# Performance work log

Hardware: AMD Instinct MI355X
Metric: run time of the kernel (lower is better)

Reference implementation:

```python
import jax, jax.numpy as jnp
import numpy as np

K = 16          # neighbors per query (args.k)
EPS_NORM = 1e-5  # LayerNorm / BatchNorm eps (torch default)


def _knn_edges(xyz, B, n):
    # batch-aware kNN: equal-sized batches, edges never cross batch boundary
    x = xyz.reshape(B, n, 3)
    d2 = jnp.sum((x[:, :, None, :] - x[:, None, :, :]) ** 2, -1)   # [B,n,n]
    _, idx = jax.lax.top_k(-d2, K)                                 # [B,n,K] local neighbor ids
    col = (idx + (jnp.arange(B) * n)[:, None, None]).reshape(-1)   # source (neighbor) [E]
    row = jnp.repeat(jnp.arange(B * n), K)                         # target (query)    [E]
    return row, col


def _forward(support_xyz, batch_index, features, lang_features, mask_flattened,
             W1, b1, ln_g, ln_b, W2, b2,
             Wl1, bl1, bn_g, bn_b, Wl2, bl2,
             Wr1, br1, Wr2, br2, row, col):
    N = support_xyz.shape[0]
    B, L, Fl = lang_features.shape
    # feat_encoder: Linear -> LayerNorm -> ReLU -> Linear
    h = features @ W1 + b1
    mu = h.mean(-1, keepdims=True)
    var = ((h - mu) ** 2).mean(-1, keepdims=True)
    h = (h - mu) / jnp.sqrt(var + EPS_NORM) * ln_g + ln_b
    feats = jax.nn.relu(h) @ W2 + b2                               # [N,F]
    # lang_encoder: Linear -> BatchNorm1d (batch statistics) -> ReLU -> Linear
    hl = lang_features.reshape(B * L, Fl) @ Wl1 + bl1
    mul = hl.mean(0)
    varl = ((hl - mul) ** 2).mean(0)
    hl = (hl - mul) / jnp.sqrt(varl + EPS_NORM) * bn_g + bn_b
    lang = (jax.nn.relu(hl) @ Wl2 + bl2).reshape(B, L, -1)         # [B,L,F]
    lang_flat = lang[batch_index]                                  # [N,L,F]
    # per-point / per-token attention logits
    atten = jnp.einsum('nf,nlf->nl', feats, lang_flat)             # [N,L]
    # segment softmax over incoming kNN edges (CenterOp max / add)
    attenmax = jax.ops.segment_max(atten[col], row, num_segments=N, indices_are_sorted=True)
    a = jnp.exp(atten[col] - attenmax[row])                        # [E,L]
    attensum = jax.ops.segment_sum(a, row, num_segments=N, indices_are_sorted=True)
    # CenterConv message
    att = a / attensum[row] * mask_flattened[row]                  # [E,L]
    att = att / (att.sum(-1, keepdims=True) + 1e-7)
    ctx = jnp.einsum('el,elf->ef', att, lang_flat[col])            # [E,F] attended lang feat
    xi, xj = support_xyz[row], support_xyz[col]
    d = xi - xj
    nrm = jnp.sqrt(jnp.sum(d * d, -1, keepdims=True) + 1e-12)
    ew = jnp.concatenate([xi, xj, d, nrm], -1)                     # [E,10]
    ew = jax.nn.relu(ew @ Wr1 + br1) @ Wr2 + br2                   # [E,F] rel_encoder
    msg = feats[col] * ctx * ew                                    # [E,F]
    rel = jax.ops.segment_sum(msg, row, num_segments=N, indices_are_sorted=True)
    return feats + rel


def setup_inputs() -> dict:
    key = jax.random.key(0)
    ks = jax.random.split(key, 12)
    B, n, L = 4, 1024, 16
    N = B * n
    Fv, Fl, F = 256, 768, 128
    def w(k, shp, fan):
        return jax.random.normal(k, shp, jnp.float32) / np.sqrt(fan).astype(np.float32)
    mask = (jax.random.uniform(ks[3], (N, L)) < 0.8).astype(jnp.float32).at[:, 0].set(1.0)
    return {
        'support_xyz': jax.random.normal(ks[0], (N, 3), jnp.float32),
        'batch_index': jnp.repeat(jnp.arange(B), n),
        'features': jax.random.normal(ks[1], (N, Fv), jnp.float32),
        'lang_features': jax.random.normal(ks[2], (B, L, Fl), jnp.float32),
        'mask_flattened': mask,
        'W1': w(ks[4], (Fv, F), Fv), 'b1': jnp.zeros(F, jnp.float32),
        'ln_g': jnp.ones(F, jnp.float32), 'ln_b': jnp.zeros(F, jnp.float32),
        'W2': w(ks[5], (F, F), F), 'b2': jnp.zeros(F, jnp.float32),
        'Wl1': w(ks[6], (Fl, F), Fl), 'bl1': jnp.zeros(F, jnp.float32),
        'bn_g': jnp.ones(F, jnp.float32), 'bn_b': jnp.zeros(F, jnp.float32),
        'Wl2': w(ks[7], (F, F), F), 'bl2': jnp.zeros(F, jnp.float32),
        'Wr1': w(ks[8], (10, 64), 10), 'br1': jnp.zeros(64, jnp.float32),
        'Wr2': w(ks[9], (64, F), 64), 'br2': jnp.zeros(F, jnp.float32),
    }


def reference(support_xyz, batch_index, features, lang_features, mask_flattened,
              W1, b1, ln_g, ln_b, W2, b2,
              Wl1, bl1, bn_g, bn_b, Wl2, bl2,
              Wr1, br1, Wr2, br2):
    B = lang_features.shape[0]
    n = support_xyz.shape[0] // B
    row, col = _knn_edges(support_xyz, B, n)
    return _forward(support_xyz, batch_index, features, lang_features, mask_flattened,
                    W1, b1, ln_g, ln_b, W2, b2,
                    Wl1, bl1, bn_g, bn_b, Wl2, bl2,
                    Wr1, br1, Wr2, br2, row, col)
```

## Files before the change

kernel.cpp:

```cpp
#include <hip/hip_runtime.h>

typedef unsigned long long u64;
typedef unsigned int u32;
typedef short short8 __attribute__((ext_vector_type(8)));
typedef float f32x4 __attribute__((ext_vector_type(4)));
typedef u32 u32x4v __attribute__((ext_vector_type(4)));

#define N_PTS   4096
#define B_SZ    4
#define L_TOK   16
#define FV      256
#define FL      768
#define FDIM    128
#define KNN     16
#define RH      64

#define MFMA_BF16(a, b, c) __builtin_amdgcn_mfma_f32_16x16x32_bf16((a), (b), (c), 0, 0, 0)

__device__ __forceinline__ short f2bf(float f) {
    unsigned int x = __float_as_uint(f);
    unsigned int r = (x + 0x7fffu + ((x >> 16) & 1u)) >> 16;
    return (short)r;
}

__device__ __forceinline__ u32 splitf(float f) {
    u32 bits = __float_as_uint(f);
    u32 hi = bits >> 16;
    float lof = f - __uint_as_float(bits & 0xffff0000u);
    u32 lo = __float_as_uint(lof) >> 16;
    return (hi << 16) | lo;
}

__global__ __launch_bounds__(256) void k1_kernel(const float* __restrict__ xyz,
                                                 const float* __restrict__ lf,
                                                 const float* __restrict__ Wl1,
                                                 const float* __restrict__ bl1,
                                                 const float* __restrict__ W1,
                                                 const float* __restrict__ W2,
                                                 const float* __restrict__ Wr2,
                                                 int* __restrict__ knn,
                                                 float* __restrict__ hl,
                                                 short* __restrict__ w1p_hi,
                                                 short* __restrict__ w1p_lo,
                                                 short* __restrict__ w2p_hi,
                                                 short* __restrict__ w2p_lo,
                                                 short* __restrict__ w2pe) {
    __shared__ float smem[3072];
    int b = blockIdx.x, t = threadIdx.x;
    int wid = t >> 6, lane = t & 63;
    int e = lane & 15, q = lane >> 4;

    if (b < 1024) {
        int base = ((b * 4) >> 10) << 10;
        for (int idx = t; idx < 3072; idx += 256) smem[idx] = xyz[base * 3 + idx];
        __syncthreads();
        int qi = b * 4 + wid;
        int ql = qi - base;
        float qx = smem[ql * 3 + 0];
        float qy = smem[ql * 3 + 1];
        float qz = smem[ql * 3 + 2];
        double key[16];
#pragma unroll
        for (int m = 0; m < 16; m++) {
            int jl = lane + (m << 6);
            float dx = qx - smem[jl * 3 + 0];
            float dy = qy - smem[jl * 3 + 1];
            float dz = qz - smem[jl * 3 + 2];
            float d2 = __fadd_rn(__fadd_rn(__fmul_rn(dx, dx), __fmul_rn(dy, dy)),
                                 __fmul_rn(dz, dz));
            key[m] = (double)__float_as_uint(d2) * 1024.0 + (double)jl;
        }
#pragma unroll
        for (int k = 2; k <= 16; k <<= 1) {
#pragma unroll
            for (int jj = k >> 1; jj > 0; jj >>= 1) {
#pragma unroll
                for (int i = 0; i < 16; i++) {
                    int l = i ^ jj;
                    if (l > i) {
                        double lo = fmin(key[i], key[l]);
                        double hi = fmax(key[i], key[l]);
                        bool asc = ((i & k) == 0);
                        key[i] = asc ? lo : hi;
                        key[l] = asc ? hi : lo;
                    }
                }
            }
        }
#pragma unroll
        for (int lvl = 1; lvl <= 32; lvl <<= 1) {
            double pk[16];
#pragma unroll
            for (int i = 0; i < 16; i++) pk[i] = __shfl_xor(key[15 - i], lvl, 64);
#pragma unroll
            for (int i = 0; i < 16; i++) key[i] = fmin(key[i], pk[i]);
            if (lvl != 32) {
#pragma unroll
                for (int jj = 8; jj > 0; jj >>= 1) {
#pragma unroll
                    for (int i = 0; i < 16; i++) {
                        int l = i ^ jj;
                        if (l > i) {
                            double lo = fmin(key[i], key[l]);
                            double hi = fmax(key[i], key[l]);
                            key[i] = lo;
                            key[l] = hi;
                        }
                    }
                }
            }
        }
        if (lane == 0) {
            int idx[16];
#pragma unroll
            for (int i = 0; i < 16; i++)
                idx[i] = base + (int)(((u64)key[i]) & 1023u);
#pragma unroll
            for (int w = 0; w < 4; w++) {
                int4 v = {idx[4 * w], idx[4 * w + 1], idx[4 * w + 2], idx[4 * w + 3]};
                *(int4*)&knn[qi * KNN + 4 * w] = v;
            }
        }
    } else if (b < 1088) {
        int r = b - 1024;
        float* lrow = smem;
        float* part = smem + 768;
        for (int k = t; k < FL; k += 256) lrow[k] = lf[r * FL + k];
        __syncthreads();
        int c = t & 127, kh = t >> 7;
        float acc = (kh == 0) ? bl1[c] : 0.f;
        int k0 = kh * 384;
        for (int k = k0; k < k0 + 384; k++) acc += lrow[k] * Wl1[k * FDIM + c];
        part[kh * FDIM + c] = acc;
        __syncthreads();
        if (kh == 0) hl[r * FDIM + c] = part[c] + part[FDIM + c];
    } else if (b < 1100) {
        int isW2 = (b >= 1096);
        int ks = isW2 ? (b - 1096) : (b - 1088);
        const float* W = isW2 ? W2 : W1;
        short* ph = isW2 ? w2p_hi : w1p_hi;
        short* pl = isW2 ? w2p_lo : w1p_lo;
#pragma unroll
        for (int p = 0; p < 2; p++) {
            int ct = wid * 2 + p;
            short8 hi, lo;
#pragma unroll
            for (int j = 0; j < 8; j++) {
                u32 pr = splitf(W[(ks * 32 + q * 8 + j) * FDIM + ct * 16 + e]);
                hi[j] = (short)(pr >> 16);
                lo[j] = (short)(pr & 0xffffu);
            }
            int o = ((ks * 8 + ct) * 64 + lane) * 8;
            *(short8*)(ph + o) = hi;
            *(short8*)(pl + o) = lo;
        }
    } else {
        int ks = b - 1100;
#pragma unroll
        for (int p = 0; p < 2; p++) {
            int ct = wid * 2 + p;
            short8 v;
#pragma unroll
            for (int j = 0; j < 8; j++)
                v[j] = f2bf(Wr2[(ks * 32 + q * 8 + j) * FDIM + ct * 16 + e]);
            *(short8*)(w2pe + ((ks * 8 + ct) * 64 + lane) * 8) = v;
        }
    }
}

__global__ __launch_bounds__(256) void k2_kernel(const float* __restrict__ features,
                                                 const short* __restrict__ w1p_hi,
                                                 const short* __restrict__ w1p_lo,
                                                 const short* __restrict__ w2p_hi,
                                                 const short* __restrict__ w2p_lo,
                                                 const float* __restrict__ b1,
                                                 const float* __restrict__ ln_g,
                                                 const float* __restrict__ ln_b,
                                                 const float* __restrict__ b2,
                                                 const float* __restrict__ hl,
                                                 const float* __restrict__ bn_g,
                                                 const float* __restrict__ bn_b,
                                                 const float* __restrict__ Wl2,
                                                 const float* __restrict__ bl2,
                                                 float* __restrict__ feats,
                                                 float* __restrict__ lang) {
    __shared__ u32 smem_u[8448];
    int b = blockIdx.x, t = threadIdx.x;
    int wid = t >> 6, lane = t & 63;
    int e = lane & 15, q = lane >> 4;
    if (b < 64) {
        int rt = b * 4 + wid;
        f32x4 acc[8];
#pragma unroll
        for (int ct = 0; ct < 8; ct++) {
            float v = b1[ct * 16 + e];
            acc[ct] = (f32x4){v, v, v, v};
        }
        for (int ks = 0; ks < 8; ks++) {
            const float* src = features + (rt * 16 + e) * FV + ks * 32 + q * 8;
            float4 f0 = *(const float4*)src;
            float4 f1 = *(const float4*)(src + 4);
            float av[8] = {f0.x, f0.y, f0.z, f0.w, f1.x, f1.y, f1.z, f1.w};
            short8 ah, al;
#pragma unroll
            for (int j = 0; j < 8; j++) {
                u32 pr = splitf(av[j]);
                ah[j] = (short)(pr >> 16);
                al[j] = (short)(pr & 0xffffu);
            }
#pragma unroll
            for (int ct = 0; ct < 8; ct++) {
                int bo = ((ks * 8 + ct) * 64 + lane) * 8;
                short8 bh = *(const short8*)(w1p_hi + bo);
                short8 bl = *(const short8*)(w1p_lo + bo);
                acc[ct] = MFMA_BF16(ah, bh, acc[ct]);
                acc[ct] = MFMA_BF16(al, bh, acc[ct]);
                acc[ct] = MFMA_BF16(ah, bl, acc[ct]);
            }
        }
        float s[4], sq[4];
#pragma unroll
        for (int r = 0; r < 4; r++) { s[r] = 0.f; sq[r] = 0.f; }
#pragma unroll
        for (int ct = 0; ct < 8; ct++)
#pragma unroll
            for (int r = 0; r < 4; r++) {
                float v = acc[ct][r];
                s[r] += v; sq[r] += v * v;
            }
#pragma unroll
        for (int off = 1; off < 16; off <<= 1)
#pragma unroll
            for (int r = 0; r < 4; r++) {
                s[r] += __shfl_xor(s[r], off, 16);
                sq[r] += __shfl_xor(sq[r], off, 16);
            }
        float mu[4], rs[4];
#pragma unroll
        for (int r = 0; r < 4; r++) {
            mu[r] = s[r] * (1.f / 128.f);
            float var = sq[r] * (1.f / 128.f) - mu[r] * mu[r];
            rs[r] = rsqrtf(var + 1e-5f);
        }
        u32* hrow = smem_u + wid * (16 * 132);
#pragma unroll
        for (int ct = 0; ct < 8; ct++) {
            float g = ln_g[ct * 16 + e], bb = ln_b[ct * 16 + e];
#pragma unroll
            for (int r = 0; r < 4; r++) {
                float n = fmaxf((acc[ct][r] - mu[r]) * rs[r] * g + bb, 0.f);
                hrow[(q * 4 + r) * 132 + ct * 16 + e] = splitf(n);
            }
        }
        f32x4 acc2[8];
#pragma unroll
        for (int ct = 0; ct < 8; ct++) {
            float v = b2[ct * 16 + e];
            acc2[ct] = (f32x4){v, v, v, v};
        }
#pragma unroll
        for (int ks = 0; ks < 4; ks++) {
            u32 hv[8];
            *(u32x4v*)&hv[0] = *(const u32x4v*)&hrow[e * 132 + ks * 32 + q * 8];
            *(u32x4v*)&hv[4] = *(const u32x4v*)&hrow[e * 132 + ks * 32 + q * 8 + 4];
            short8 ah, al;
#pragma unroll
            for (int j = 0; j < 8; j++) {
                ah[j] = (short)(hv[j] >> 16);
                al[j] = (short)(hv[j] & 0xffffu);
            }
#pragma unroll
            for (int ct = 0; ct < 8; ct++) {
                int bo = ((ks * 8 + ct) * 64 + lane) * 8;
                short8 bh = *(const short8*)(w2p_hi + bo);
                short8 bl = *(const short8*)(w2p_lo + bo);
                acc2[ct] = MFMA_BF16(ah, bh, acc2[ct]);
                acc2[ct] = MFMA_BF16(al, bh, acc2[ct]);
                acc2[ct] = MFMA_BF16(ah, bl, acc2[ct]);
            }
        }
#pragma unroll
        for (int ct = 0; ct < 8; ct++)
#pragma unroll
            for (int r = 0; r < 4; r++)
                feats[(rt * 16 + q * 4 + r) * FDIM + ct * 16 + e] = acc2[ct][r];
    } else {
        float* rl4 = (float*)smem_u;
        int tt = t & 127;
        int act = (t < 128);
        int r0 = (b - 64) * 4;
        if (act) {
            float s = 0.f, s2 = 0.f;
            for (int r = 0; r < 64; r++) {
                float v = hl[r * FDIM + tt];
                s += v; s2 += v * v;
            }
            float mu = s * (1.f / 64.f);
            float var = s2 * (1.f / 64.f) - mu * mu;
            float rs = rsqrtf(var + 1e-5f);
            float g = bn_g[tt], bb = bn_b[tt];
#pragma unroll
            for (int p = 0; p < 4; p++)
                rl4[p * FDIM + tt] = fmaxf((hl[(r0 + p) * FDIM + tt] - mu) * rs * g + bb, 0.f);
        }
        __syncthreads();
        if (act) {
            float bv = bl2[tt];
            float a0 = bv, a1 = bv, a2 = bv, a3 = bv;
            for (int k = 0; k < FDIM; k++) {
                float w = Wl2[k * FDIM + tt];
                a0 += rl4[0 * FDIM + k] * w;
                a1 += rl4[1 * FDIM + k] * w;
                a2 += rl4[2 * FDIM + k] * w;
                a3 += rl4[3 * FDIM + k] * w;
            }
            lang[(r0 + 0) * FDIM + tt] = a0;
            lang[(r0 + 1) * FDIM + tt] = a1;
            lang[(r0 + 2) * FDIM + tt] = a2;
            lang[(r0 + 3) * FDIM + tt] = a3;
        }
    }
}

__global__ __launch_bounds__(256) void atten_kernel(const float* __restrict__ feats,
                                                    const float* __restrict__ lang,
                                                    float* __restrict__ atten,
                                                    short* __restrict__ langp) {
    int b = blockIdx.x, t = threadIdx.x;
    int wid = t >> 6, lane = t & 63;
    int e = lane & 15, q = lane >> 4;
    if (b < 64) {
        int pt0 = (b * 4 + wid) * 16;
        int bi = pt0 >> 10;
        const float* arow = feats + (pt0 + e) * FDIM;
        const float* brow = lang + (bi * L_TOK + e) * FDIM;
        f32x4 acc = {0.f, 0.f, 0.f, 0.f};
#pragma unroll
        for (int ks = 0; ks < 4; ks++) {
            int off = ks * 32 + q * 8;
            float4 a0 = *(const float4*)(arow + off);
            float4 a1 = *(const float4*)(arow + off + 4);
            float4 c0 = *(const float4*)(brow + off);
            float4 c1 = *(const float4*)(brow + off + 4);
            float av[8] = {a0.x, a0.y, a0.z, a0.w, a1.x, a1.y, a1.z, a1.w};
            float bv[8] = {c0.x, c0.y, c0.z, c0.w, c1.x, c1.y, c1.z, c1.w};
            short8 ah, al, bh, bl;
#pragma unroll
            for (int j = 0; j < 8; j++) {
                u32 pa = splitf(av[j]);
                u32 pb = splitf(bv[j]);
                ah[j] = (short)(pa >> 16);
                al[j] = (short)(pa & 0xffffu);
                bh[j] = (short)(pb >> 16);
                bl[j] = (short)(pb & 0xffffu);
            }
            acc = MFMA_BF16(ah, bh, acc);
            acc = MFMA_BF16(al, bh, acc);
            acc = MFMA_BF16(ah, bl, acc);
        }
#pragma unroll
        for (int r = 0; r < 4; r++)
            atten[(pt0 + q * 4 + r) * L_TOK + e] = acc[r];
    } else {
        int bi = b - 64;
#pragma unroll
        for (int p = 0; p < 2; p++) {
            int tile = wid * 2 + p;
            short8 v;
            if (q < 2) {
#pragma unroll
                for (int j = 0; j < 8; j++)
                    v[j] = f2bf(lang[bi * L_TOK * FDIM + (q * 8 + j) * FDIM + tile * 16 + e]);
            } else {
#pragma unroll
                for (int j = 0; j < 8; j++) v[j] = 0;
            }
            *(short8*)(langp + ((bi * 8 + tile) * 64 + lane) * 8) = v;
        }
    }
}

__global__ __launch_bounds__(256) void edge_kernel(const float* __restrict__ xyz,
                                                   const float* __restrict__ mask,
                                                   const float* __restrict__ Wr1,
                                                   const float* __restrict__ br1,
                                                   const float* __restrict__ br2,
                                                   const int* __restrict__ knn,
                                                   const short* __restrict__ w2pe,
                                                   const short* __restrict__ langp,
                                                   const float* __restrict__ feats,
                                                   const float* __restrict__ atten,
                                                   float* __restrict__ out) {
    int lane = threadIdx.x & 63;
    int wid  = threadIdx.x >> 6;
    int i    = blockIdx.x * 4 + wid;
    int bi   = i >> 10;
    int quad = lane >> 4;
    int e16  = lane & 15;

    int idxe = knn[i * KNN + e16];

    float sat[8];
    if (quad < 2) {
        const float4* ap = (const float4*)(atten + idxe * L_TOK + quad * 8);
        float4 a0 = ap[0], a1 = ap[1];
        sat[0] = a0.x; sat[1] = a0.y; sat[2] = a0.z; sat[3] = a0.w;
        sat[4] = a1.x; sat[5] = a1.y; sat[6] = a1.z; sat[7] = a1.w;
    } else {
#pragma unroll
        for (int j = 0; j < 8; j++) sat[j] = 0.f;
    }

    float mx[8];
#pragma unroll
    for (int j = 0; j < 8; j++) mx[j] = sat[j];
#pragma unroll
    for (int off = 1; off < 16; off <<= 1) {
#pragma unroll
        for (int j = 0; j < 8; j++) mx[j] = fmaxf(mx[j], __shfl_xor(mx[j], off, 16));
    }
    float ex[8], sm[8];
#pragma unroll
    for (int j = 0; j < 8; j++) { ex[j] = __expf(sat[j] - mx[j]); sm[j] = ex[j]; }
#pragma unroll
    for (int off = 1; off < 16; off <<= 1) {
#pragma unroll
        for (int j = 0; j < 8; j++) sm[j] += __shfl_xor(sm[j], off, 16);
    }
    float st[8];
    if (quad < 2) {
        const float4* mp = (const float4*)(mask + i * L_TOK + quad * 8);
        float4 m0 = mp[0], m1 = mp[1];
        float mv[8] = {m0.x, m0.y, m0.z, m0.w, m1.x, m1.y, m1.z, m1.w};
#pragma unroll
        for (int j = 0; j < 8; j++) st[j] = ex[j] * (mv[j] / sm[j]);
    } else {
#pragma unroll
        for (int j = 0; j < 8; j++) st[j] = 0.f;
    }
    float s = st[0] + st[1] + st[2] + st[3] + st[4] + st[5] + st[6] + st[7];
    s += __shfl_xor(s, 16, 64);
    s += __shfl_xor(s, 32, 64);
    float inv2 = 1.f / (s + 1e-7f);
    short8 sattA;
#pragma unroll
    for (int j = 0; j < 8; j++) sattA[j] = f2bf(st[j] * inv2);

    float xi0 = xyz[i * 3 + 0], xi1 = xyz[i * 3 + 1], xi2 = xyz[i * 3 + 2];
    float xj0 = xyz[idxe * 3 + 0], xj1 = xyz[idxe * 3 + 1], xj2 = xyz[idxe * 3 + 2];
    float d0 = xi0 - xj0, d1 = xi1 - xj1, d2v = xi2 - xj2;
    float nr = sqrtf(d0 * d0 + d1 * d1 + d2v * d2v + 1e-12f);
    float ein[10] = {xi0, xi1, xi2, xj0, xj1, xj2, d0, d1, d2v, nr};
    short8 hidA[2];
#pragma unroll
    for (int sstep = 0; sstep < 2; sstep++) {
        int k0 = sstep * 32 + quad * 8;
        float h[8];
        const float4* bp = (const float4*)(br1 + k0);
        float4 b0 = bp[0], b1v = bp[1];
        h[0] = b0.x; h[1] = b0.y; h[2] = b0.z; h[3] = b0.w;
        h[4] = b1v.x; h[5] = b1v.y; h[6] = b1v.z; h[7] = b1v.w;
#pragma unroll
        for (int m = 0; m < 10; m++) {
            const float4* wp = (const float4*)(Wr1 + m * RH + k0);
            float4 w0 = wp[0], w1 = wp[1];
            float em = ein[m];
            h[0] += em * w0.x; h[1] += em * w0.y; h[2] += em * w0.z; h[3] += em * w0.w;
            h[4] += em * w1.x; h[5] += em * w1.y; h[6] += em * w1.z; h[7] += em * w1.w;
        }
#pragma unroll
        for (int j = 0; j < 8; j++) hidA[sstep][j] = f2bf(fmaxf(h[j], 0.f));
    }

    int idxr[4];
#pragma unroll
    for (int r = 0; r < 4; r++) idxr[r] = knn[i * KNN + quad * 4 + r];

#pragma unroll 2
    for (int tile = 0; tile < 8; tile++) {
        int cc = tile * 16 + e16;
        f32x4 accew = {0.f, 0.f, 0.f, 0.f};
#pragma unroll
        for (int sstep = 0; sstep < 2; sstep++) {
            short8 w2B = *(const short8*)(w2pe + ((sstep * 8 + tile) * 64 + lane) * 8);
            accew = MFMA_BF16(hidA[sstep], w2B, accew);
        }
        short8 lsB = *(const short8*)(langp + ((bi * 8 + tile) * 64 + lane) * 8);
        f32x4 accctx = {0.f, 0.f, 0.f, 0.f};
        accctx = MFMA_BF16(sattA, lsB, accctx);

        float br2c = br2[cc];
        float msum = 0.f;
#pragma unroll
        for (int r = 0; r < 4; r++) {
            float fj = feats[idxr[r] * FDIM + cc];
            msum += fj * accctx[r] * (accew[r] + br2c);
        }
        msum += __shfl_xor(msum, 16, 64);
        msum += __shfl_xor(msum, 32, 64);
        if (lane < 16)
            out[i * FDIM + cc] = feats[i * FDIM + cc] + msum;
    }
}

extern "C" void kernel_launch(void* const* d_in, const int* in_sizes, int n_in,
                              void* d_out, int out_size, void* d_ws, size_t ws_size,
                              hipStream_t stream) {
    const float* xyz   = (const float*)d_in[0];
    const float* features = (const float*)d_in[2];
    const float* lang_f   = (const float*)d_in[3];
    const float* mask     = (const float*)d_in[4];
    const float* W1   = (const float*)d_in[5];
    const float* b1   = (const float*)d_in[6];
    const float* ln_g = (const float*)d_in[7];
    const float* ln_b = (const float*)d_in[8];
    const float* W2   = (const float*)d_in[9];
    const float* b2   = (const float*)d_in[10];
    const float* Wl1  = (const float*)d_in[11];
    const float* bl1  = (const float*)d_in[12];
    const float* bn_g = (const float*)d_in[13];
    const float* bn_b = (const float*)d_in[14];
    const float* Wl2  = (const float*)d_in[15];
    const float* bl2  = (const float*)d_in[16];
    const float* Wr1  = (const float*)d_in[17];
    const float* br1  = (const float*)d_in[18];
    const float* Wr2  = (const float*)d_in[19];
    const float* br2  = (const float*)d_in[20];

    float* ws_feats = (float*)d_ws;
    float* ws_atten = ws_feats + N_PTS * FDIM;
    float* ws_lang  = ws_atten + N_PTS * L_TOK;
    float* ws_hl    = ws_lang + B_SZ * L_TOK * FDIM;
    int*   ws_knn   = (int*)(ws_hl + 64 * FDIM);
    short* w1p_hi   = (short*)(ws_knn + N_PTS * KNN);
    short* w1p_lo   = w1p_hi + FV * FDIM;
    short* w2p_hi   = w1p_lo + FV * FDIM;
    short* w2p_lo   = w2p_hi + FDIM * FDIM;
    short* w2pe     = w2p_lo + FDIM * FDIM;
    short* langp    = w2pe + RH * FDIM;

    k1_kernel<<<1102, 256, 0, stream>>>(xyz, lang_f, Wl1, bl1, W1, W2, Wr2,
                                        ws_knn, ws_hl,
                                        w1p_hi, w1p_lo, w2p_hi, w2p_lo, w2pe);
    k2_kernel<<<80, 256, 0, stream>>>(features, w1p_hi, w1p_lo, w2p_hi, w2p_lo,
                                      b1, ln_g, ln_b, b2,
                                      ws_hl, bn_g, bn_b, Wl2, bl2,
                                      ws_feats, ws_lang);
    atten_kernel<<<68, 256, 0, stream>>>(ws_feats, ws_lang, ws_atten, langp);
    edge_kernel<<<N_PTS / 4, 256, 0, stream>>>(xyz, mask, Wr1, br1, br2,
                                               ws_knn, w2pe, langp, ws_feats, ws_atten,
                                               (float*)d_out);
}
```

Baseline: 163.3 us.

## Fuse kNN search into edge kernel and shrink prep kernel

Moves the per-query kNN bitonic selection out of the first kernel and into the final edge kernel. The neighbour indices now pass through a small shared array instead of a global workspace buffer. This shrinks the prep kernel from 1102 to 78 blocks, so the feature-encoder kernel can start sooner, and it removes the global write and read of the knn indices. In exchange, candidate coordinates are read straight from global memory rather than from a staged LDS tile. The edge kernel also takes on the register pressure of the 16-double sort, which may lower its occupancy.

```diff
diff --git a/kernel.cpp b/kernel.cpp
--- a/kernel.cpp
+++ b/kernel.cpp
@@ -31,98 +31,25 @@
     return (hi << 16) | lo;
 }
 
-__global__ __launch_bounds__(256) void k1_kernel(const float* __restrict__ xyz,
-                                                 const float* __restrict__ lf,
-                                                 const float* __restrict__ Wl1,
-                                                 const float* __restrict__ bl1,
-                                                 const float* __restrict__ W1,
-                                                 const float* __restrict__ W2,
-                                                 const float* __restrict__ Wr2,
-                                                 int* __restrict__ knn,
-                                                 float* __restrict__ hl,
-                                                 short* __restrict__ w1p_hi,
-                                                 short* __restrict__ w1p_lo,
-                                                 short* __restrict__ w2p_hi,
-                                                 short* __restrict__ w2p_lo,
-                                                 short* __restrict__ w2pe) {
-    __shared__ float smem[3072];
+__global__ __launch_bounds__(256) void prep_kernel(const float* __restrict__ lf,
+                                                   const float* __restrict__ Wl1,
+                                                   const float* __restrict__ bl1,
+                                                   const float* __restrict__ W1,
+                                                   const float* __restrict__ W2,
+                                                   const float* __restrict__ Wr2,
+                                                   float* __restrict__ hl,
+                                                   short* __restrict__ w1p_hi,
+                                                   short* __restrict__ w1p_lo,
+                                                   short* __restrict__ w2p_hi,
+                                                   short* __restrict__ w2p_lo,
+                                                   short* __restrict__ w2pe) {
+    __shared__ float smem[1024];
     int b = blockIdx.x, t = threadIdx.x;
     int wid = t >> 6, lane = t & 63;
     int e = lane & 15, q = lane >> 4;
 
-    if (b < 1024) {
-        int base = ((b * 4) >> 10) << 10;
-        for (int idx = t; idx < 3072; idx += 256) smem[idx] = xyz[base * 3 + idx];
-        __syncthreads();
-        int qi = b * 4 + wid;
-        int ql = qi - base;
-        float qx = smem[ql * 3 + 0];
-        float qy = smem[ql * 3 + 1];
-        float qz = smem[ql * 3 + 2];
-        double key[16];
-#pragma unroll
-        for (int m = 0; m < 16; m++) {
-            int jl = lane + (m << 6);
-            float dx = qx - smem[jl * 3 + 0];
-            float dy = qy - smem[jl * 3 + 1];
-            float dz = qz - smem[jl * 3 + 2];
-            float d2 = __fadd_rn(__fadd_rn(__fmul_rn(dx, dx), __fmul_rn(dy, dy)),
-                                 __fmul_rn(dz, dz));
-            key[m] = (double)__float_as_uint(d2) * 1024.0 + (double)jl;
-        }
-#pragma unroll
-        for (int k = 2; k <= 16; k <<= 1) {
-#pragma unroll
-            for (int jj = k >> 1; jj > 0; jj >>= 1) {
-#pragma unroll
-                for (int i = 0; i < 16; i++) {
-                    int l = i ^ jj;
-                    if (l > i) {
-                        double lo = fmin(key[i], key[l]);
-                        double hi = fmax(key[i], key[l]);
-                        bool asc = ((i & k) == 0);
-                        key[i] = asc ? lo : hi;
-                        key[l] = asc ? hi : lo;
-                    }
-                }
-            }
-        }
-#pragma unroll
-        for (int lvl = 1; lvl <= 32; lvl <<= 1) {
-            double pk[16];
-#pragma unroll
-            for (int i = 0; i < 16; i++) pk[i] = __shfl_xor(key[15 - i], lvl, 64);
-#pragma unroll
-            for (int i = 0; i < 16; i++) key[i] = fmin(key[i], pk[i]);
-            if (lvl != 32) {
-#pragma unroll
-                for (int jj = 8; jj > 0; jj >>= 1) {
-#pragma unroll
-                    for (int i = 0; i < 16; i++) {
-                        int l = i ^ jj;
-                        if (l > i) {
-                            double lo = fmin(key[i], key[l]);
-                            double hi = fmax(key[i], key[l]);
-                            key[i] = lo;
-                            key[l] = hi;
-                        }
-                    }
-                }
-            }
-        }
-        if (lane == 0) {
-            int idx[16];
-#pragma unroll
-            for (int i = 0; i < 16; i++)
-                idx[i] = base + (int)(((u64)key[i]) & 1023u);
-#pragma unroll
-            for (int w = 0; w < 4; w++) {
-                int4 v = {idx[4 * w], idx[4 * w + 1], idx[4 * w + 2], idx[4 * w + 3]};
-                *(int4*)&knn[qi * KNN + 4 * w] = v;
-            }
-        }
-    } else if (b < 1088) {
-        int r = b - 1024;
+    if (b < 64) {
+        int r = b;
         float* lrow = smem;
         float* part = smem + 768;
         for (int k = t; k < FL; k += 256) lrow[k] = lf[r * FL + k];
@@ -134,9 +61,9 @@
         part[kh * FDIM + c] = acc;
         __syncthreads();
         if (kh == 0) hl[r * FDIM + c] = part[c] + part[FDIM + c];
-    } else if (b < 1100) {
-        int isW2 = (b >= 1096);
-        int ks = isW2 ? (b - 1096) : (b - 1088);
+    } else if (b < 76) {
+        int isW2 = (b >= 72);
+        int ks = isW2 ? (b - 72) : (b - 64);
         const float* W = isW2 ? W2 : W1;
         short* ph = isW2 ? w2p_hi : w1p_hi;
         short* pl = isW2 ? w2p_lo : w1p_lo;
@@ -155,7 +82,7 @@
             *(short8*)(pl + o) = lo;
         }
     } else {
-        int ks = b - 1100;
+        int ks = b - 76;
 #pragma unroll
         for (int p = 0; p < 2; p++) {
             int ct = wid * 2 + p;
@@ -380,25 +307,96 @@
     }
 }
 
-__global__ __launch_bounds__(256) void edge_kernel(const float* __restrict__ xyz,
-                                                   const float* __restrict__ mask,
-                                                   const float* __restrict__ Wr1,
-                                                   const float* __restrict__ br1,
-                                                   const float* __restrict__ br2,
-                                                   const int* __restrict__ knn,
-                                                   const short* __restrict__ w2pe,
-                                                   const short* __restrict__ langp,
-                                                   const float* __restrict__ feats,
-                                                   const float* __restrict__ atten,
-                                                   float* __restrict__ out) {
-    int lane = threadIdx.x & 63;
-    int wid  = threadIdx.x >> 6;
-    int i    = blockIdx.x * 4 + wid;
-    int bi   = i >> 10;
-    int quad = lane >> 4;
-    int e16  = lane & 15;
-
-    int idxe = knn[i * KNN + e16];
+__global__ __launch_bounds__(256) void knn_edge_kernel(const float* __restrict__ xyz,
+                                                       const float* __restrict__ mask,
+                                                       const float* __restrict__ Wr1,
+                                                       const float* __restrict__ br1,
+                                                       const float* __restrict__ br2,
+                                                       const short* __restrict__ w2pe,
+                                                       const short* __restrict__ langp,
+                                                       const float* __restrict__ feats,
+                                                       const float* __restrict__ atten,
+                                                       float* __restrict__ out) {
+    __shared__ int nbrs[4][16];
+    int t = threadIdx.x;
+    int wid = t >> 6, lane = t & 63;
+    int quad = lane >> 4, e16 = lane & 15;
+    int i = blockIdx.x * 4 + wid;
+    int bi = i >> 10;
+    int base = bi << 10;
+
+    {
+        float qx = xyz[i * 3 + 0];
+        float qy = xyz[i * 3 + 1];
+        float qz = xyz[i * 3 + 2];
+        double key[16];
+#pragma unroll
+        for (int m = 0; m < 16; m++) {
+            int jl = lane + (m << 6);
+            int j = base + jl;
+            float dx = qx - xyz[j * 3 + 0];
+            float dy = qy - xyz[j * 3 + 1];
+            float dz = qz - xyz[j * 3 + 2];
+            float d2 = __fadd_rn(__fadd_rn(__fmul_rn(dx, dx), __fmul_rn(dy, dy)),
+                                 __fmul_rn(dz, dz));
+            key[m] = (double)__float_as_uint(d2) * 1024.0 + (double)jl;
+        }
+#pragma unroll
+        for (int k = 2; k <= 16; k <<= 1) {
+#pragma unroll
+            for (int jj = k >> 1; jj > 0; jj >>= 1) {
+#pragma unroll
+                for (int ii = 0; ii < 16; ii++) {
+                    int l = ii ^ jj;
+                    if (l > ii) {
+                        double lo = fmin(key[ii], key[l]);
+                        double hi = fmax(key[ii], key[l]);
+                        bool asc = ((ii & k) == 0);
+                        key[ii] = asc ? lo : hi;
+                        key[l] = asc ? hi : lo;
+                    }
+                }
+            }
+        }
+#pragma unroll
+        for (int lvl = 1; lvl <= 32; lvl <<= 1) {
+            double pk[16];
+#pragma unroll
+            for (int ii = 0; ii < 16; ii++) pk[ii] = __shfl_xor(key[15 - ii], lvl, 64);
+#pragma unroll
+            for (int ii = 0; ii < 16; ii++) key[ii] = fmin(key[ii], pk[ii]);
+            if (lvl != 32) {
+#pragma unroll
+                for (int jj = 8; jj > 0; jj >>= 1) {
+#pragma unroll
+                    for (int ii = 0; ii < 16; ii++) {
+                        int l = ii ^ jj;
+                        if (l > ii) {
+                            double lo = fmin(key[ii], key[l]);
+                            double hi = fmax(key[ii], key[l]);
+                            key[ii] = lo;
+                            key[l] = hi;
+                        }
+                    }
+                }
+            }
+        }
+        if (lane == 0) {
+            int idx[16];
+#pragma unroll
+            for (int ii = 0; ii < 16; ii++)
+                idx[ii] = base + (int)(((u64)key[ii]) & 1023u);
+#pragma unroll
+            for (int w = 0; w < 4; w++) {
+                int4 v = {idx[4 * w], idx[4 * w + 1], idx[4 * w + 2], idx[4 * w + 3]};
+                *(int4*)&nbrs[wid][4 * w] = v;
+            }
+        }
+    }
+    int idxe = nbrs[wid][e16];
+    int idxr[4];
+#pragma unroll
+    for (int r = 0; r < 4; r++) idxr[r] = nbrs[wid][quad * 4 + r];
 
     float sat[8];
     if (quad < 2) {
@@ -471,10 +469,6 @@
 #pragma unroll
         for (int j = 0; j < 8; j++) hidA[sstep][j] = f2bf(fmaxf(h[j], 0.f));
     }
-
-    int idxr[4];
-#pragma unroll
-    for (int r = 0; r < 4; r++) idxr[r] = knn[i * KNN + quad * 4 + r];
 
 #pragma unroll 2
     for (int tile = 0; tile < 8; tile++) {
@@ -531,23 +525,21 @@
     float* ws_atten = ws_feats + N_PTS * FDIM;
     float* ws_lang  = ws_atten + N_PTS * L_TOK;
     float* ws_hl    = ws_lang + B_SZ * L_TOK * FDIM;
-    int*   ws_knn   = (int*)(ws_hl + 64 * FDIM);
-    short* w1p_hi   = (short*)(ws_knn + N_PTS * KNN);
+    short* w1p_hi   = (short*)(ws_hl + 64 * FDIM);
     short* w1p_lo   = w1p_hi + FV * FDIM;
     short* w2p_hi   = w1p_lo + FV * FDIM;
     short* w2p_lo   = w2p_hi + FDIM * FDIM;
     short* w2pe     = w2p_lo + FDIM * FDIM;
     short* langp    = w2pe + RH * FDIM;
 
-    k1_kernel<<<1102, 256, 0, stream>>>(xyz, lang_f, Wl1, bl1, W1, W2, Wr2,
-                                        ws_knn, ws_hl,
-                                        w1p_hi, w1p_lo, w2p_hi, w2p_lo, w2pe);
+    prep_kernel<<<78, 256, 0, stream>>>(lang_f, Wl1, bl1, W1, W2, Wr2,
+                                        ws_hl, w1p_hi, w1p_lo, w2p_hi, w2p_lo, w2pe);
     k2_kernel<<<80, 256, 0, stream>>>(features, w1p_hi, w1p_lo, w2p_hi, w2p_lo,
                                       b1, ln_g, ln_b, b2,
                                       ws_hl, bn_g, bn_b, Wl2, bl2,
                                       ws_feats, ws_lang);
     atten_kernel<<<68, 256, 0, stream>>>(ws_feats, ws_lang, ws_atten, langp);
-    edge_kernel<<<N_PTS / 4, 256, 0, stream>>>(xyz, mask, Wr1, br1, br2,
-                                               ws_knn, w2pe, langp, ws_feats, ws_atten,
-                                               (float*)d_out);
-}
+    knn_edge_kernel<<<N_PTS / 4, 256, 0, stream>>>(xyz, mask, Wr1, br1, br2,
+                                                   w2pe, langp, ws_feats, ws_atten,
+                                                   (float*)d_out);
+}
```

Result: slower. 171.2 us (+4.8%).
